# Optimization experiments

Hardware: AMD Instinct MI355X
Metric: run time of the kernel (lower is better)

The kernel has to match this reference:

```python
import jax, jax.numpy as jnp
import numpy as np

N = 30000   # nodes
E = 120000  # edges
G = 512     # graphs in batch
F_IN = 1
H1 = 32
H2 = 64
NC = 10


def _lin_init(key, fan_in, fan_out):
    s = 1.0 / np.sqrt(fan_in)
    kw, kb = jax.random.split(key)
    w = jax.random.uniform(kw, (fan_in, fan_out), jnp.float32, minval=-s, maxval=s)
    b = jax.random.uniform(kb, (fan_out,), jnp.float32, minval=-s, maxval=s)
    return w, b


def setup_inputs() -> dict:
    key = jax.random.key(0)
    ks = jax.random.split(key, 16)
    inp = {}
    inp["x"] = jax.random.normal(ks[0], (N, F_IN), jnp.float32)
    inp["edge_attr"] = jax.random.uniform(ks[1], (E, 2), jnp.float32)
    inp["pos"] = jax.random.uniform(ks[2], (N, 2), jnp.float32) * 27.0
    inp["w1a"], inp["b1a"] = _lin_init(ks[3], 2, 25)
    inp["w1b"], inp["b1b"] = _lin_init(ks[4], 25, F_IN * H1)
    inp["root1"], inp["bias1"] = _lin_init(ks[5], F_IN, H1)
    inp["w2a"], inp["b2a"] = _lin_init(ks[6], 2, 25)
    inp["w2b"], inp["b2b"] = _lin_init(ks[7], 25, H1 * H2)
    inp["root2"], inp["bias2"] = _lin_init(ks[8], H1, H2)
    inp["fc1_w"], inp["fc1_b"] = _lin_init(ks[9], H2, 128)
    inp["fc2_w"], inp["fc2_b"] = _lin_init(ks[10], 128, NC)
    inp["edge_index"] = jax.random.randint(ks[11], (2, E), 0, N)
    inp["batch"] = jnp.sort(jax.random.randint(ks[12], (N,), 0, G))
    return inp


def _seg_mean(v, idx, n):
    s = jax.ops.segment_sum(v, idx, num_segments=n)
    c = jax.ops.segment_sum(jnp.ones((v.shape[0], 1), v.dtype), idx, num_segments=n)
    return s / jnp.maximum(c, 1.0)


def _nnconv(x, src, dst, ea, wa, ba, wb, bb, root, bias, n_seg, n_out):
    # per-edge weight matrix from edge MLP: [E, f_in, f_out]
    f_in, f_out = root.shape
    W = (jax.nn.relu(ea @ wa + ba) @ wb + bb).reshape(-1, f_in, f_out)
    msg = jnp.einsum('ei,eio->eo', x[src], W)          # gather + per-edge matmul
    aggr = _seg_mean(msg, dst, n_seg)[:n_out]          # mean scatter-reduce
    return aggr + x @ root + bias


def _forward(x, edge_attr, pos, w1a, b1a, w1b, b1b, root1, bias1,
             w2a, b2a, w2b, b2b, root2, bias2, fc1_w, fc1_b, fc2_w, fc2_b,
             edge_index, batch):
    row, col = edge_index[0], edge_index[1]
    h = jax.nn.elu(_nnconv(x, row, col, edge_attr, w1a, b1a, w1b, b1b,
                           root1, bias1, N, N))
    # graclus stand-in: fixed pairwise matching (consecutive cluster ids)
    n2 = N // 2
    cluster1 = jnp.arange(N) // 2
    x2 = jax.ops.segment_max(h, cluster1, num_segments=n2)     # max_pool x
    pos2 = _seg_mean(pos, cluster1, n2)                        # pool_pos (mean)
    batch2 = batch[0::2]                                       # pool_batch via perm
    row2 = cluster1[row]
    col2 = cluster1[col]
    mask = row2 != col2                                        # drop self loops
    col2m = jnp.where(mask, col2, n2)                          # route to dummy seg
    cart = (pos2[col2] - pos2[row2]) * mask[:, None]           # cartesian pseudo
    max_v = jnp.abs(cart).max()
    ea2 = cart / (2.0 * max_v) + 0.5
    h2 = jax.nn.elu(_nnconv(x2, row2, col2m, ea2, w2a, b2a, w2b, b2b,
                            root2, bias2, n2 + 1, n2))
    n3 = n2 // 2
    cluster2 = jnp.arange(n2) // 2
    x3 = jax.ops.segment_max(h2, cluster2, num_segments=n3)    # max_pool_x
    batch3 = batch2[0::2]
    g = _seg_mean(x3, batch3, G)                               # global_mean_pool
    g = jax.nn.elu(g @ fc1_w + fc1_b)                          # dropout off (eval)
    return jax.nn.log_softmax(g @ fc2_w + fc2_b, axis=1)


def reference(x, edge_attr, pos, w1a, b1a, w1b, b1b, root1, bias1,
              w2a, b2a, w2b, b2b, root2, bias2, fc1_w, fc1_b, fc2_w, fc2_b,
              edge_index, batch):
    return _forward(x, edge_attr, pos, w1a, b1a, w1b, b1b, root1, bias1,
                    w2a, b2a, w2b, b2b, root2, bias2, fc1_w, fc1_b,
                    fc2_w, fc2_b, edge_index, batch)
```

## Files before the change

### kernel.cpp

```cpp
#include <hip/hip_runtime.h>
#include <hip/hip_bf16.h>

#define N_NODES 30000
#define N_EDGES 120000
#define NGRAPH  512
#define N2      15000
#define N3      7500
#define NC      10

#define TSN   4
#define NTS   (N2 / TSN)
#define EC4   64
#define NB1   32
#define NBLK1 ((N_NODES + NB1 - 1) / NB1)
#define EC1   128
#define NDEGB ((N_EDGES + 255) / 256)

#define SC_C1 118
#define SC_C2 59
#define SC_CS 15
#define SC_CT (SC_C1 + SC_C2 + SC_CS)

typedef __hip_bfloat16 bf16;

__device__ __forceinline__ float lo(const float* p, int i) { return p[i]; }
__device__ __forceinline__ float lo(const bf16* p, int i) { return __bfloat162float(p[i]); }
__device__ __forceinline__ void sto(float* p, int i, float v) { p[i] = v; }
__device__ __forceinline__ void sto(bf16* p, int i, float v) { p[i] = __float2bfloat16(v); }
__device__ __forceinline__ float elu(float x) { return x > 0.f ? x : expm1f(x); }

#define MV_OFF    0
#define GS_OFF    1
#define GC_OFF    32769
#define DEG1_OFF  33281
#define DEG2_OFF  63281
#define DEGS_OFF  78281
#define ZERO_FLOATS 82031
#define OFF1_OFF  82031
#define CUR1_OFF  112032
#define OFF2_OFF  142032
#define CUR2_OFF  157033
#define OFFS_OFF  172033
#define CURS_OFF  175784
#define BSUM_OFF  179534
#define ES1_OFF   179726
#define ESS_OFF   299726
#define DPOS_OFF  419726
#define X2_OFF    539726
#define P2_OFF    1019726
#define CT_OFF    1049726
#define MSG_OFF   1289726
#define FLAG_OFF  8969726

struct K1Smem {
  float tl2[EC1][28];
  float axl[EC1], ayl[EC1];
  float xsl[EC1];
  float w1a[50];
  float b1a[25];
  float b1b[32];
  float r1[32];
  float bs1[32];
  float hbuf[NB1][33];
  int offl[NB1 + 1];
};

struct K4Smem {
  float YT[TSN][64][36];
  float tl[EC4][28];
  float xl[TSN][32];
  float w2a[50];
  float b2a[25];
  float axl[EC4], ayl[EC4];
  int dpl[EC4];
  int nll[EC4];
};

struct K5Smem {
  float r2l[2048];
  float b2l[64];
  float hl[4][64];
};

__global__ __launch_bounds__(256) void kc_deg(
    const int* __restrict__ ei, const void* x, const void* ea, int* __restrict__ flag,
    int* __restrict__ deg1, int* __restrict__ deg2, int* __restrict__ degS) {
  if (blockIdx.x == NDEGB) {
    const bf16* xb = (const bf16*)x;
    const bf16* eb = (const bf16*)ea;
    int tid = threadIdx.x;
    float a = __bfloat162float(xb[tid]);
    float b = __bfloat162float(eb[tid]);
    int bad = (!(fabsf(a) < 1e3f)) || (!(fabsf(b) < 1e3f));
    unsigned long long m = __ballot(bad);
    __shared__ int anyb[4];
    int w = tid >> 6;
    if ((tid & 63) == 0) anyb[w] = (m != 0ULL) ? 1 : 0;
    __syncthreads();
    if (tid == 0) flag[0] = (anyb[0] | anyb[1] | anyb[2] | anyb[3]);
    return;
  }
  int e = blockIdx.x * 256 + threadIdx.x;
  if (e >= N_EDGES) return;
  int row = ei[e], col = ei[N_EDGES + e];
  atomicAdd(deg1 + col, 1);
  int r2 = row >> 1, c2 = col >> 1;
  if (r2 != c2) {
    atomicAdd(deg2 + c2, 1);
    atomicAdd(degS + (r2 >> 2), 1);
  }
}

__global__ __launch_bounds__(256) void ks_scanA(
    const int* __restrict__ deg1, const int* __restrict__ deg2, const int* __restrict__ degS,
    int* __restrict__ off1, int* __restrict__ off2, int* __restrict__ offS,
    int* __restrict__ bsum) {
  __shared__ int buf[256];
  int c = blockIdx.x, tid = threadIdx.x;
  const int* deg; int* off; int n, local;
  if (c < SC_C1)              { deg = deg1; off = off1; n = 30000; local = c; }
  else if (c < SC_C1 + SC_C2) { deg = deg2; off = off2; n = 15000; local = c - SC_C1; }
  else                        { deg = degS; off = offS; n = 3750;  local = c - SC_C1 - SC_C2; }
  int i = local * 256 + tid;
  int v = (i < n) ? deg[i] : 0;
  buf[tid] = v;
  __syncthreads();
  for (int s = 1; s < 256; s <<= 1) {
    int t = (tid >= s) ? buf[tid - s] : 0;
    __syncthreads();
    buf[tid] += t;
    __syncthreads();
  }
  if (i <= n) off[i] = buf[tid] - v;
  if (tid == 255) bsum[c] = buf[255];
}

__global__ __launch_bounds__(256) void ks_scanB(int* __restrict__ bsum) {
  __shared__ int buf[256];
  int a = blockIdx.x, tid = threadIdx.x;
  int nc, cb;
  if (a == 0)      { nc = SC_C1; cb = 0; }
  else if (a == 1) { nc = SC_C2; cb = SC_C1; }
  else             { nc = SC_CS; cb = SC_C1 + SC_C2; }
  int v = (tid < nc) ? bsum[cb + tid] : 0;
  buf[tid] = v;
  __syncthreads();
  for (int s = 1; s < 256; s <<= 1) {
    int t = (tid >= s) ? buf[tid - s] : 0;
    __syncthreads();
    buf[tid] += t;
    __syncthreads();
  }
  if (tid < nc) bsum[cb + tid] = buf[tid] - v;
}

__global__ __launch_bounds__(256) void ks_scanC(
    int* __restrict__ off1, int* __restrict__ off2, int* __restrict__ offS,
    int* __restrict__ cur1, int* __restrict__ cur2, int* __restrict__ curS,
    const int* __restrict__ bsum) {
  int c = blockIdx.x, tid = threadIdx.x;
  int* off; int* cur; int n, local;
  if (c < SC_C1)              { off = off1; cur = cur1; n = 30000; local = c; }
  else if (c < SC_C1 + SC_C2) { off = off2; cur = cur2; n = 15000; local = c - SC_C1; }
  else                        { off = offS; cur = curS; n = 3750;  local = c - SC_C1 - SC_C2; }
  int add = bsum[c];
  int i = local * 256 + tid;
  if (i <= n) off[i] += add;
  if (i < n) cur[i] = off[i];
}

__global__ __launch_bounds__(256) void kc_place(const int* __restrict__ ei,
                                                int* __restrict__ cur1, int* __restrict__ es1,
                                                int* __restrict__ cur2, int* __restrict__ dpos,
                                                int* __restrict__ curS, int* __restrict__ ess) {
  int e = blockIdx.x * 256 + threadIdx.x;
  if (e >= N_EDGES) return;
  int row = ei[e], col = ei[N_EDGES + e];
  int p = atomicAdd(cur1 + col, 1);
  es1[p] = e;
  int r2 = row >> 1, c2 = col >> 1;
  if (r2 != c2) {
    int q = atomicAdd(cur2 + c2, 1);
    dpos[e] = q;
    int u = atomicAdd(curS + (r2 >> 2), 1);
    ess[u] = e;
  }
}

template <typename T>
__device__ void k1_impl(K1Smem& S,
    const T* __restrict__ x, const T* __restrict__ ea, const T* __restrict__ pos,
    const int* __restrict__ ei,
    const T* __restrict__ w1a, const T* __restrict__ b1a,
    const T* __restrict__ w1b, const T* __restrict__ b1b,
    const T* __restrict__ root1, const T* __restrict__ bias1,
    const int* __restrict__ off1, const int* __restrict__ es1,
    float* __restrict__ x2, float* __restrict__ pos2) {
  int tid = threadIdx.x, t = blockIdx.x;
  int n0 = t * NB1;
  for (int j = tid; j < 50; j += 256) S.w1a[j] = lo(w1a, j);
  for (int j = tid; j < 25; j += 256) S.b1a[j] = lo(b1a, j);
  if (tid < 32) {
    S.b1b[tid] = lo(b1b, tid);
    S.r1[tid] = lo(root1, tid);
    S.bs1[tid] = lo(bias1, tid);
  }
  if (tid <= NB1) {
    int n = n0 + tid; if (n > N_NODES) n = N_NODES;
    S.offl[tid] = off1[n];
  }
  int wv = tid >> 6, lane = tid & 63, o = lane & 31, hf = lane >> 5;
  float wreg[28];
#pragma unroll
  for (int k = 0; k < 25; ++k) wreg[k] = lo(w1b, k * 32 + o);
  wreg[25] = wreg[26] = wreg[27] = 0.f;
  __syncthreads();
  int jbeg = S.offl[0], jend = S.offl[NB1];
  float bb = S.b1b[o];
  float acc[8];
#pragma unroll
  for (int s = 0; s < 8; ++s) acc[s] = 0.f;
  for (int jb = jbeg; jb < jend; jb += EC1) {
    int ecnt = jend - jb; if (ecnt > EC1) ecnt = EC1;
    __syncthreads();
    if (tid < ecnt) {
      int e = es1[jb + tid];
      S.axl[tid] = lo(ea, 2 * e);
      S.ayl[tid] = lo(ea, 2 * e + 1);
      S.xsl[tid] = lo(x, ei[e]);
    }
    __syncthreads();
    for (int idx = tid; idx < ecnt * 32; idx += 256) {
      int j = idx >> 5, k = idx & 31;
      if (k < 25)
        S.tl2[j][k] = fmaxf(S.axl[j] * S.w1a[k] + S.ayl[j] * S.w1a[25 + k] + S.b1a[k], 0.f);
      else if (k < 28)
        S.tl2[j][k] = 0.f;
    }
    __syncthreads();
#pragma unroll
    for (int s = 0; s < 8; ++s) {
      int nl = wv + 4 * s;
      int lj = S.offl[nl]; if (lj < jb) lj = jb;
      int hj = S.offl[nl + 1]; if (hj > jb + ecnt) hj = jb + ecnt;
      for (int j = lj + hf; j < hj; j += 2) {
        int sj = j - jb;
        const float4* tq4 = (const float4*)S.tl2[sj];
        float m0 = bb, m1 = 0.f, m2 = 0.f, m3 = 0.f;
#pragma unroll
        for (int q = 0; q < 7; ++q) {
          float4 tv = tq4[q];
          m0 += tv.x * wreg[4 * q];
          m1 += tv.y * wreg[4 * q + 1];
          m2 += tv.z * wreg[4 * q + 2];
          m3 += tv.w * wreg[4 * q + 3];
        }
        acc[s] += S.xsl[sj] * ((m0 + m1) + (m2 + m3));
      }
    }
  }
#pragma unroll
  for (int s = 0; s < 8; ++s) {
    int nl = wv + 4 * s;
    float a = acc[s] + __shfl_xor(acc[s], 32, 64);
    int n = n0 + nl;
    if (hf == 0 && n < N_NODES) {
      float c = (float)(S.offl[nl + 1] - S.offl[nl]);
      c = fmaxf(c, 1.f);
      S.hbuf[nl][o] = elu(a / c + lo(x, n) * S.r1[o] + S.bs1[o]);
    }
  }
  __syncthreads();
  for (int idx = tid; idx < (NB1 / 2) * 32; idx += 256) {
    int pl = idx >> 5, oo = idx & 31;
    int m = t * (NB1 / 2) + pl;
    if (m < N2)
      x2[m * 32 + oo] = fmaxf(S.hbuf[2 * pl][oo], S.hbuf[2 * pl + 1][oo]);
  }
  if (tid < NB1) {
    int pl = tid >> 1, c = tid & 1;
    int m = t * (NB1 / 2) + pl;
    if (m < N2)
      pos2[m * 2 + c] = 0.5f * (lo(pos, (2 * m) * 2 + c) + lo(pos, (2 * m + 1) * 2 + c));
  }
}

__global__ __launch_bounds__(256, 4) void k1_both(
    const int* __restrict__ flag,
    const void* x, const void* ea, const void* pos, const int* ei,
    const void* w1a, const void* b1a, const void* w1b, const void* b1b,
    const void* root1, const void* bias1,
    const int* off1, const int* es1, float* x2, float* pos2) {
  extern __shared__ char sm1[];
  K1Smem& S = *reinterpret_cast<K1Smem*>(sm1);
  if (flag[0] == 1)
    k1_impl<float>(S, (const float*)x, (const float*)ea, (const float*)pos, ei,
                   (const float*)w1a, (const float*)b1a, (const float*)w1b, (const float*)b1b,
                   (const float*)root1, (const float*)bias1, off1, es1, x2, pos2);
  else
    k1_impl<bf16>(S, (const bf16*)x, (const bf16*)ea, (const bf16*)pos, ei,
                  (const bf16*)w1a, (const bf16*)b1a, (const bf16*)w1b, (const bf16*)b1b,
                  (const bf16*)root1, (const bf16*)bias1, off1, es1, x2, pos2);
}

__global__ __launch_bounds__(256) void k3_cart(
    const int* __restrict__ ei, const float* __restrict__ pos2,
    float* __restrict__ cart, unsigned int* __restrict__ maxv) {
  int e = blockIdx.x * 256 + threadIdx.x;
  float m = 0.f;
  if (e < N_EDGES) {
    int r2 = ei[e] >> 1, c2 = ei[N_EDGES + e] >> 1;
    float cx = 0.f, cy = 0.f;
    if (r2 != c2) {
      cx = pos2[2 * c2] - pos2[2 * r2];
      cy = pos2[2 * c2 + 1] - pos2[2 * r2 + 1];
    }
    cart[2 * e] = cx;
    cart[2 * e + 1] = cy;
    m = fmaxf(fabsf(cx), fabsf(cy));
  }
#pragma unroll
  for (int s = 32; s > 0; s >>= 1)
    m = fmaxf(m, __shfl_xor(m, s, 64));
  __shared__ float wm[4];
  int lane = threadIdx.x & 63, wid = threadIdx.x >> 6;
  if (lane == 0) wm[wid] = m;
  __syncthreads();
  if (threadIdx.x == 0) {
    float mm = fmaxf(fmaxf(wm[0], wm[1]), fmaxf(wm[2], wm[3]));
    atomicMax(maxv, __float_as_uint(mm));
  }
}

template <typename T>
__device__ void k4_impl(K4Smem& S,
    const int* __restrict__ ei, const float* __restrict__ cart, const float* __restrict__ maxv_f,
    const float* __restrict__ x2,
    const T* __restrict__ w2a, const T* __restrict__ b2a,
    const T* __restrict__ w2b, const T* __restrict__ b2b,
    const int* __restrict__ offS, const int* __restrict__ ess,
    const int* __restrict__ dpos, float* __restrict__ msg) {
  int tid = threadIdx.x, t = blockIdx.x;
  int n0 = t * TSN;
  if (tid < TSN * 32) S.xl[tid >> 5][tid & 31] = x2[n0 * 32 + tid];
  for (int j = tid; j < 50; j += 256) S.w2a[j] = lo(w2a, j);
  for (int j = tid; j < 25; j += 256) S.b2a[j] = lo(b2a, j);
  __syncthreads();
  int w = tid >> 6, o = tid & 63;
  for (int kk = w; kk < 28; kk += 4) {
    float a0 = 0.f, a1 = 0.f, a2 = 0.f, a3 = 0.f;
    if (kk < 26) {
      const T* srcp = (kk < 25) ? (w2b + kk * 2048) : b2b;
#pragma unroll 8
      for (int i = 0; i < 32; ++i) {
        float q = lo(srcp, i * 64 + o);
        a0 += S.xl[0][i] * q;
        a1 += S.xl[1][i] * q;
        a2 += S.xl[2][i] * q;
        a3 += S.xl[3][i] * q;
      }
    }
    S.YT[0][o][kk] = a0; S.YT[1][o][kk] = a1;
    S.YT[2][o][kk] = a2; S.YT[3][o][kk] = a3;
  }
  float inv = 0.5f / maxv_f[0];
  int j0 = offS[t], j1 = offS[t + 1];
  for (int jb = j0; jb < j1; jb += EC4) {
    int ecnt = j1 - jb; if (ecnt > EC4) ecnt = EC4;
    __syncthreads();
    if (tid < ecnt) {
      int e = ess[jb + tid];
      int r2 = ei[e] >> 1;
      S.nll[tid] = r2 & (TSN - 1);
      S.dpl[tid] = dpos[e];
      S.axl[tid] = cart[2 * e] * inv + 0.5f;
      S.ayl[tid] = cart[2 * e + 1] * inv + 0.5f;
    }
    __syncthreads();
    for (int idx = tid; idx < ecnt * 32; idx += 256) {
      int j = idx >> 5, k = idx & 31;
      if (k < 25)
        S.tl[j][k] = fmaxf(S.axl[j] * S.w2a[k] + S.ayl[j] * S.w2a[25 + k] + S.b2a[k], 0.f);
      else if (k < 28)
        S.tl[j][k] = (k == 25) ? 1.f : 0.f;
    }
    __syncthreads();
    for (int j = w; j < ecnt; j += 4) {
      const float4* yq = (const float4*)&S.YT[S.nll[j]][o][0];
      const float4* tq = (const float4*)S.tl[j];
      float a0 = 0.f, a1 = 0.f, a2 = 0.f, a3 = 0.f;
#pragma unroll
      for (int q = 0; q < 7; ++q) {
        float4 tv = tq[q], yv = yq[q];
        a0 += tv.x * yv.x; a1 += tv.y * yv.y;
        a2 += tv.z * yv.z; a3 += tv.w * yv.w;
      }
      msg[(size_t)S.dpl[j] * 64 + o] = (a0 + a1) + (a2 + a3);
    }
  }
}

__global__ __launch_bounds__(256, 3) void k4_both(
    const int* __restrict__ flag,
    const int* ei, const float* cart, const float* maxv_f, const float* x2,
    const void* w2a, const void* b2a, const void* w2b, const void* b2b,
    const int* offS, const int* ess, const int* dpos, float* msg) {
  extern __shared__ char sm4[];
  K4Smem& S = *reinterpret_cast<K4Smem*>(sm4);
  if (flag[0] == 1)
    k4_impl<float>(S, ei, cart, maxv_f, x2, (const float*)w2a, (const float*)b2a,
                   (const float*)w2b, (const float*)b2b, offS, ess, dpos, msg);
  else
    k4_impl<bf16>(S, ei, cart, maxv_f, x2, (const bf16*)w2a, (const bf16*)b2a,
                  (const bf16*)w2b, (const bf16*)b2b, offS, ess, dpos, msg);
}

template <typename T>
__device__ void k5_impl(K5Smem& S,
    const float* __restrict__ msg, const int* __restrict__ off2,
    const float* __restrict__ x2,
    const T* __restrict__ root2, const T* __restrict__ bias2,
    const int* __restrict__ batch,
    float* __restrict__ gsum, float* __restrict__ gcnt) {
  int tid = threadIdx.x;
  for (int j = tid; j < 2048; j += 256) S.r2l[j] = lo(root2, j);
  if (tid < 64) S.b2l[tid] = lo(bias2, tid);
  __syncthreads();
  int w = tid >> 6, o = tid & 63;
  int d = blockIdx.x * 4 + w;
  int j0 = off2[d], j1 = off2[d + 1];
  float s0 = 0.f, s1 = 0.f;
  int j = j0;
  for (; j + 1 < j1; j += 2) {
    s0 += msg[(size_t)j * 64 + o];
    s1 += msg[(size_t)(j + 1) * 64 + o];
  }
  if (j < j1) s0 += msg[(size_t)j * 64 + o];
  float c = fmaxf((float)(j1 - j0), 1.f);
  float r = S.b2l[o];
  const float* xr = x2 + d * 32;
#pragma unroll 8
  for (int i = 0; i < 32; ++i) r += xr[i] * S.r2l[i * 64 + o];
  S.hl[w][o] = elu((s0 + s1) / c + r);
  __syncthreads();
  if (tid < 128) {
    int p = tid >> 6, oo = tid & 63;
    float v = fmaxf(S.hl[2 * p][oo], S.hl[2 * p + 1][oo]);
    int m = blockIdx.x * 2 + p;
    int g = batch[4 * m];
    atomicAdd(gsum + g * 64 + oo, v);
    if (oo == 0) atomicAdd(gcnt + g, 1.f);
  }
}

__global__ __launch_bounds__(256) void k5_both(
    const int* __restrict__ flag,
    const float* msg, const int* off2, const float* x2,
    const void* root2, const void* bias2, const int* batch,
    float* gsum, float* gcnt) {
  extern __shared__ char sm5[];
  K5Smem& S = *reinterpret_cast<K5Smem*>(sm5);
  if (flag[0] == 1)
    k5_impl<float>(S, msg, off2, x2, (const float*)root2, (const float*)bias2, batch, gsum, gcnt);
  else
    k5_impl<bf16>(S, msg, off2, x2, (const bf16*)root2, (const bf16*)bias2, batch, gsum, gcnt);
}

template <typename T>
__device__ void k7_impl(const float* __restrict__ gsum, const float* __restrict__ gcnt,
                        const T* __restrict__ fc1_w, const T* __restrict__ fc1_b,
                        const T* __restrict__ fc2_w, const T* __restrict__ fc2_b,
                        T* __restrict__ out) {
  __shared__ float gv[64];
  __shared__ float h1s[128];
  __shared__ float zs[NC];
  __shared__ float lse;
  int g = blockIdx.x, tid = threadIdx.x;
  if (tid < 64) gv[tid] = gsum[g * 64 + tid] / fmaxf(gcnt[g], 1.f);
  __syncthreads();
  float a = lo(fc1_b, tid);
#pragma unroll 8
  for (int o = 0; o < 64; ++o) a += gv[o] * lo(fc1_w, o * 128 + tid);
  h1s[tid] = elu(a);
  __syncthreads();
  if (tid < NC) {
    float s = lo(fc2_b, tid);
    for (int j = 0; j < 128; ++j) s += h1s[j] * lo(fc2_w, j * NC + tid);
    zs[tid] = s;
  }
  __syncthreads();
  if (tid == 0) {
    float m = -1e30f;
    for (int c = 0; c < NC; ++c) m = fmaxf(m, zs[c]);
    float s = 0.f;
    for (int c = 0; c < NC; ++c) s += expf(zs[c] - m);
    lse = m + logf(s);
  }
  __syncthreads();
  if (tid < NC) sto(out, g * NC + tid, zs[tid] - lse);
}

__global__ __launch_bounds__(128) void k7_both(
    const int* __restrict__ flag,
    const float* gsum, const float* gcnt,
    const void* fc1_w, const void* fc1_b, const void* fc2_w, const void* fc2_b,
    void* out) {
  if (flag[0] == 1)
    k7_impl<float>(gsum, gcnt, (const float*)fc1_w, (const float*)fc1_b,
                   (const float*)fc2_w, (const float*)fc2_b, (float*)out);
  else
    k7_impl<bf16>(gsum, gcnt, (const bf16*)fc1_w, (const bf16*)fc1_b,
                  (const bf16*)fc2_w, (const bf16*)fc2_b, (bf16*)out);
}

extern "C" void kernel_launch(void* const* d_in, const int* in_sizes, int n_in,
                              void* d_out, int out_size, void* d_ws, size_t ws_size,
                              hipStream_t stream) {
  float* ws = (float*)d_ws;
  const int* flag = (const int*)(ws + FLAG_OFF);
  const int* ei = (const int*)d_in[19];
  const int* batch = (const int*)d_in[20];

  hipMemsetAsync(d_ws, 0, (size_t)ZERO_FLOATS * 4, stream);

  kc_deg<<<NDEGB + 1, 256, 0, stream>>>(
      ei, d_in[0], d_in[1], (int*)(ws + FLAG_OFF),
      (int*)(ws + DEG1_OFF), (int*)(ws + DEG2_OFF), (int*)(ws + DEGS_OFF));
  ks_scanA<<<SC_CT, 256, 0, stream>>>(
      (const int*)(ws + DEG1_OFF), (const int*)(ws + DEG2_OFF), (const int*)(ws + DEGS_OFF),
      (int*)(ws + OFF1_OFF), (int*)(ws + OFF2_OFF), (int*)(ws + OFFS_OFF),
      (int*)(ws + BSUM_OFF));
  ks_scanB<<<3, 256, 0, stream>>>((int*)(ws + BSUM_OFF));
  ks_scanC<<<SC_CT, 256, 0, stream>>>(
      (int*)(ws + OFF1_OFF), (int*)(ws + OFF2_OFF), (int*)(ws + OFFS_OFF),
      (int*)(ws + CUR1_OFF), (int*)(ws + CUR2_OFF), (int*)(ws + CURS_OFF),
      (const int*)(ws + BSUM_OFF));
  kc_place<<<NDEGB, 256, 0, stream>>>(
      ei, (int*)(ws + CUR1_OFF), (int*)(ws + ES1_OFF),
      (int*)(ws + CUR2_OFF), (int*)(ws + DPOS_OFF),
      (int*)(ws + CURS_OFF), (int*)(ws + ESS_OFF));

  k1_both<<<NBLK1, 256, sizeof(K1Smem), stream>>>(
      flag, d_in[0], d_in[1], d_in[2], ei,
      d_in[3], d_in[4], d_in[5], d_in[6], d_in[7], d_in[8],
      (const int*)(ws + OFF1_OFF), (const int*)(ws + ES1_OFF),
      ws + X2_OFF, ws + P2_OFF);

  k3_cart<<<NDEGB, 256, 0, stream>>>(
      ei, ws + P2_OFF, ws + CT_OFF, (unsigned int*)(ws + MV_OFF));

  k4_both<<<NTS, 256, sizeof(K4Smem), stream>>>(
      flag, ei, ws + CT_OFF, ws + MV_OFF, ws + X2_OFF,
      d_in[9], d_in[10], d_in[11], d_in[12],
      (const int*)(ws + OFFS_OFF), (const int*)(ws + ESS_OFF),
      (const int*)(ws + DPOS_OFF), ws + MSG_OFF);

  k5_both<<<N2 / 4, 256, sizeof(K5Smem), stream>>>(
      flag, ws + MSG_OFF, (const int*)(ws + OFF2_OFF), ws + X2_OFF,
      d_in[13], d_in[14], batch, ws + GS_OFF, ws + GC_OFF);

  k7_both<<<NGRAPH, 128, 0, stream>>>(
      flag, ws + GS_OFF, ws + GC_OFF,
      d_in[15], d_in[16], d_in[17], d_in[18], d_out);
}
```

Measured before the change: 294.2 us.

## Reassociate layer-1 edge MLP into per-node hidden sums and swizzle YT layout

The first NNConv now uses linearity: each node accumulates x_src times the hidden ReLU features (plus a bias slot) across its incoming edges, then applies w1b once per node instead of once per edge. This removes the per-edge 25x32 matvec and the shared tl2 staging pass, and the edge chunk size is doubled. Separately, the layer-2 YT shared array drops its padding to 32 columns and uses an XOR swizzle on float4 groups to avoid LDS bank conflicts, with the loop widened to 8 float4s. Floating-point summation order changes, so results may differ slightly.

```diff
diff --git a/kernel.cpp b/kernel.cpp
--- a/kernel.cpp
+++ b/kernel.cpp
@@ -13,7 +13,7 @@
 #define EC4   64
 #define NB1   32
 #define NBLK1 ((N_NODES + NB1 - 1) / NB1)
-#define EC1   128
+#define EC1   256
 #define NDEGB ((N_EDGES + 255) / 256)
 
 #define SC_C1 118
@@ -53,9 +53,8 @@
 #define FLAG_OFF  8969726
 
 struct K1Smem {
-  float tl2[EC1][28];
-  float axl[EC1], ayl[EC1];
-  float xsl[EC1];
+  float srow[NB1][28];
+  float axl[EC1], ayl[EC1], xsl[EC1];
   float w1a[50];
   float b1a[25];
   float b1b[32];
@@ -66,8 +65,8 @@
 };
 
 struct K4Smem {
-  float YT[TSN][64][36];
-  float tl[EC4][28];
+  float YT[TSN][64][32];
+  float tl[EC4][32];
   float xl[TSN][32];
   float w2a[50];
   float b2a[25];
@@ -209,17 +208,18 @@
     int n = n0 + tid; if (n > N_NODES) n = N_NODES;
     S.offl[tid] = off1[n];
   }
-  int wv = tid >> 6, lane = tid & 63, o = lane & 31, hf = lane >> 5;
+  int half = tid >> 5, lk = tid & 31;
   float wreg[28];
 #pragma unroll
-  for (int k = 0; k < 25; ++k) wreg[k] = lo(w1b, k * 32 + o);
-  wreg[25] = wreg[26] = wreg[27] = 0.f;
-  __syncthreads();
+  for (int k = 0; k < 25; ++k) wreg[k] = lo(w1b, k * 32 + lk);
+  wreg[26] = 0.f; wreg[27] = 0.f;
+  __syncthreads();
+  wreg[25] = S.b1b[lk];
+  float wa0 = 0.f, wa1 = 0.f, wb = 0.f;
+  if (lk < 25) { wa0 = S.w1a[lk]; wa1 = S.w1a[25 + lk]; wb = S.b1a[lk]; }
   int jbeg = S.offl[0], jend = S.offl[NB1];
-  float bb = S.b1b[o];
-  float acc[8];
-#pragma unroll
-  for (int s = 0; s < 8; ++s) acc[s] = 0.f;
+  int base = half * 4;
+  float s0 = 0.f, s1 = 0.f, s2 = 0.f, s3 = 0.f;
   for (int jb = jbeg; jb < jend; jb += EC1) {
     int ecnt = jend - jb; if (ecnt > EC1) ecnt = EC1;
     __syncthreads();
@@ -230,44 +230,39 @@
       S.xsl[tid] = lo(x, ei[e]);
     }
     __syncthreads();
-    for (int idx = tid; idx < ecnt * 32; idx += 256) {
-      int j = idx >> 5, k = idx & 31;
-      if (k < 25)
-        S.tl2[j][k] = fmaxf(S.axl[j] * S.w1a[k] + S.ayl[j] * S.w1a[25 + k] + S.b1a[k], 0.f);
-      else if (k < 28)
-        S.tl2[j][k] = 0.f;
-    }
-    __syncthreads();
+    int je = jb + ecnt;
+#define K1ACC(i, sacc) { \
+    int lj = S.offl[base + i]; if (lj < jb) lj = jb; \
+    int hj = S.offl[base + i + 1]; if (hj > je) hj = je; \
+    for (int j = lj; j < hj; ++j) { \
+      int sj = j - jb; \
+      float tk = (lk < 25) ? fmaxf(S.axl[sj] * wa0 + S.ayl[sj] * wa1 + wb, 0.f) : 1.f; \
+      sacc += S.xsl[sj] * tk; } }
+    K1ACC(0, s0) K1ACC(1, s1) K1ACC(2, s2) K1ACC(3, s3)
+#undef K1ACC
+  }
+  if (lk < 26) {
+    S.srow[base][lk] = s0; S.srow[base + 1][lk] = s1;
+    S.srow[base + 2][lk] = s2; S.srow[base + 3][lk] = s3;
+  } else if (lk < 28) {
+    S.srow[base][lk] = 0.f; S.srow[base + 1][lk] = 0.f;
+    S.srow[base + 2][lk] = 0.f; S.srow[base + 3][lk] = 0.f;
+  }
 #pragma unroll
-    for (int s = 0; s < 8; ++s) {
-      int nl = wv + 4 * s;
-      int lj = S.offl[nl]; if (lj < jb) lj = jb;
-      int hj = S.offl[nl + 1]; if (hj > jb + ecnt) hj = jb + ecnt;
-      for (int j = lj + hf; j < hj; j += 2) {
-        int sj = j - jb;
-        const float4* tq4 = (const float4*)S.tl2[sj];
-        float m0 = bb, m1 = 0.f, m2 = 0.f, m3 = 0.f;
+  for (int i = 0; i < 4; ++i) {
+    int nl = base + i, n = n0 + nl;
+    if (n < N_NODES) {
+      const float4* sq = (const float4*)S.srow[nl];
+      float a0 = 0.f, a1 = 0.f, a2 = 0.f, a3 = 0.f;
 #pragma unroll
-        for (int q = 0; q < 7; ++q) {
-          float4 tv = tq4[q];
-          m0 += tv.x * wreg[4 * q];
-          m1 += tv.y * wreg[4 * q + 1];
-          m2 += tv.z * wreg[4 * q + 2];
-          m3 += tv.w * wreg[4 * q + 3];
-        }
-        acc[s] += S.xsl[sj] * ((m0 + m1) + (m2 + m3));
+      for (int q = 0; q < 7; ++q) {
+        float4 sv = sq[q];
+        a0 += sv.x * wreg[4 * q];     a1 += sv.y * wreg[4 * q + 1];
+        a2 += sv.z * wreg[4 * q + 2]; a3 += sv.w * wreg[4 * q + 3];
       }
-    }
-  }
-#pragma unroll
-  for (int s = 0; s < 8; ++s) {
-    int nl = wv + 4 * s;
-    float a = acc[s] + __shfl_xor(acc[s], 32, 64);
-    int n = n0 + nl;
-    if (hf == 0 && n < N_NODES) {
       float c = (float)(S.offl[nl + 1] - S.offl[nl]);
       c = fmaxf(c, 1.f);
-      S.hbuf[nl][o] = elu(a / c + lo(x, n) * S.r1[o] + S.bs1[o]);
+      S.hbuf[nl][lk] = elu(((a0 + a1) + (a2 + a3)) / c + lo(x, n) * S.r1[lk] + S.bs1[lk]);
     }
   }
   __syncthreads();
@@ -347,7 +342,8 @@
   for (int j = tid; j < 25; j += 256) S.b2a[j] = lo(b2a, j);
   __syncthreads();
   int w = tid >> 6, o = tid & 63;
-  for (int kk = w; kk < 28; kk += 4) {
+  int ox = o & 7;
+  for (int kk = w; kk < 32; kk += 4) {
     float a0 = 0.f, a1 = 0.f, a2 = 0.f, a3 = 0.f;
     if (kk < 26) {
       const T* srcp = (kk < 25) ? (w2b + kk * 2048) : b2b;
@@ -360,8 +356,9 @@
         a3 += S.xl[3][i] * q;
       }
     }
-    S.YT[0][o][kk] = a0; S.YT[1][o][kk] = a1;
-    S.YT[2][o][kk] = a2; S.YT[3][o][kk] = a3;
+    int sk = ((((kk >> 2) ^ ox) << 2) | (kk & 3));
+    S.YT[0][o][sk] = a0; S.YT[1][o][sk] = a1;
+    S.YT[2][o][sk] = a2; S.YT[3][o][sk] = a3;
   }
   float inv = 0.5f / maxv_f[0];
   int j0 = offS[t], j1 = offS[t + 1];
@@ -381,17 +378,18 @@
       int j = idx >> 5, k = idx & 31;
       if (k < 25)
         S.tl[j][k] = fmaxf(S.axl[j] * S.w2a[k] + S.ayl[j] * S.w2a[25 + k] + S.b2a[k], 0.f);
-      else if (k < 28)
+      else
         S.tl[j][k] = (k == 25) ? 1.f : 0.f;
     }
     __syncthreads();
     for (int j = w; j < ecnt; j += 4) {
-      const float4* yq = (const float4*)&S.YT[S.nll[j]][o][0];
+      const float* yrow = &S.YT[S.nll[j]][o][0];
       const float4* tq = (const float4*)S.tl[j];
       float a0 = 0.f, a1 = 0.f, a2 = 0.f, a3 = 0.f;
 #pragma unroll
-      for (int q = 0; q < 7; ++q) {
-        float4 tv = tq[q], yv = yq[q];
+      for (int q = 0; q < 8; ++q) {
+        float4 tv = tq[q];
+        float4 yv = *(const float4*)&yrow[(q ^ ox) << 2];
         a0 += tv.x * yv.x; a1 += tv.y * yv.y;
         a2 += tv.z * yv.z; a3 += tv.w * yv.w;
       }
```

New measurement: 292.5 us. No clear change (-0.6%).
